# Kernel optimization log

Hardware: AMD Instinct MI355X
Metric: run time of the kernel (lower is better)

Reference implementation:

```python
import jax, jax.numpy as jnp
import numpy as np
from jax import lax

NUM_HEADS = 8


def setup_inputs() -> dict:
    key = jax.random.key(0)
    ks = jax.random.split(key, 6)
    B, L, Hd = 4, 4096, 512
    S = 45  # factor * ceil(ln(L)) = 5 * 9
    x = jax.random.normal(ks[0], (B, L, Hd), dtype=jnp.float32)
    scale = 1.0 / np.sqrt(Hd)
    Wq = jax.random.normal(ks[1], (Hd, Hd), dtype=jnp.float32) * scale
    Wk = jax.random.normal(ks[2], (Hd, Hd), dtype=jnp.float32) * scale
    Wv = jax.random.normal(ks[3], (Hd, Hd), dtype=jnp.float32) * scale
    Wo = jax.random.normal(ks[4], (Hd, Hd), dtype=jnp.float32) * scale
    index_sample = jax.random.randint(ks[5], (L, S), 0, L, dtype=jnp.int32)
    return {"x": x, "Wq": Wq, "Wk": Wk, "Wv": Wv, "Wo": Wo,
            "index_sample": index_sample}


def reference(x, Wq, Wk, Wv, Wo, index_sample):
    B, L, Hd = x.shape
    H = NUM_HEADS
    D = Hd // H
    S = index_sample.shape[1]
    u = S  # n_top active queries = factor*ceil(ln(L))

    def split_heads(t):  # [B,L,Hd] -> [B,H,L,D]
        return t.reshape(B, L, H, D).transpose(0, 2, 1, 3)

    q = split_heads(x @ Wq)
    k = split_heads(x @ Wk)
    v = split_heads(x @ Wv)

    scale = 1.0 / jnp.sqrt(jnp.asarray(D, dtype=x.dtype))

    # sampled key gather: [B,H,L,S,D]
    K_samp = k[:, :, index_sample, :]
    # sampled scores per query: [B,H,L,S]
    QK_samp = jnp.einsum('bhld,bhlsd->bhls', q, K_samp)
    # sparsity measurement: max - mean over sampled keys
    M = QK_samp.max(axis=-1) - QK_samp.mean(axis=-1)  # [B,H,L]
    _, top_idx = lax.top_k(M, u)                      # [B,H,u]

    # full attention only for active queries
    Qr = jnp.take_along_axis(q, top_idx[..., None], axis=2)   # [B,H,u,D]
    scores = jnp.einsum('bhud,bhld->bhul', Qr, k) * scale     # [B,H,u,L]
    attn = jax.nn.softmax(scores, axis=-1)
    ctx_sel = jnp.einsum('bhul,bhld->bhud', attn, v)          # [B,H,u,D]

    # inactive queries get mean(V); scatter active results in
    context = jnp.broadcast_to(v.mean(axis=2, keepdims=True), (B, H, L, D))
    b_idx = jnp.arange(B)[:, None, None]
    h_idx = jnp.arange(H)[None, :, None]
    context = context.at[b_idx, h_idx, top_idx].set(ctx_sel)

    out = context.transpose(0, 2, 1, 3).reshape(B, L, Hd) @ Wo
    return out
```

## Files before the change

### kernel.cpp

```cpp
#include <hip/hip_runtime.h>
#include <cmath>

#define SS 45
#define FSPLIT 16

typedef __attribute__((ext_vector_type(8))) _Float16 half8;
typedef __attribute__((ext_vector_type(4))) float float4v;
typedef __attribute__((ext_vector_type(8))) unsigned short ushort8v;

__device__ inline unsigned short f16b(float f) {
    union { _Float16 h; unsigned short u; } c;
    c.h = (_Float16)f;
    return c.u;
}
__device__ inline float f16back(unsigned short u) {
    union { _Float16 h; unsigned short u; } c;
    c.u = u;
    return (float)c.h;
}

__device__ __forceinline__ void async16(const void* g, void* l) {
    __builtin_amdgcn_global_load_lds(
        (const __attribute__((address_space(1))) void*)g,
        (__attribute__((address_space(3))) void*)l, 16, 0, 0);
}

template <int CTRL>
__device__ __forceinline__ float dppadd(float v) {
    int x = __builtin_amdgcn_mov_dpp(__float_as_int(v), CTRL, 0xF, 0xF, true);
    return v + __int_as_float(x);
}
template <int CTRL>
__device__ __forceinline__ float dppmax(float v) {
    int x = __builtin_amdgcn_mov_dpp(__float_as_int(v), CTRL, 0xF, 0xF, true);
    return fmaxf(v, __int_as_float(x));
}

__device__ __forceinline__ unsigned int fmono(float f) {
    unsigned int u = __float_as_uint(f);
    return (u & 0x80000000u) ? ~u : (u | 0x80000000u);
}

__global__ __launch_bounds__(256) void convW_kernel(
    const float* __restrict__ Wq, const float* __restrict__ Wk, const float* __restrict__ Wv,
    unsigned short* __restrict__ WTh, unsigned short* __restrict__ WTl,
    float* __restrict__ vmp)
{
    int bid = blockIdx.x;
    if (bid < 768) {
        int zy = bid >> 8;
        int bxy = bid & 255;
        const float* W = (zy == 0) ? Wq : (zy == 1) ? Wk : Wv;
        unsigned short* th = WTh + (size_t)zy * 262144;
        unsigned short* tl = WTl + (size_t)zy * 262144;
        __shared__ float t[32][33];
        int bx = bxy & 15, by = bxy >> 4;
        int tx = threadIdx.x & 31, ty = threadIdx.x >> 5;
        for (int i = ty; i < 32; i += 8) t[i][tx] = W[(size_t)(by * 32 + i) * 512 + bx * 32 + tx];
        __syncthreads();
        for (int i = ty; i < 32; i += 8) {
            float f = t[tx][i];
            unsigned short h = f16b(f);
            unsigned short lo = f16b(f - f16back(h));
            th[(size_t)(bx * 32 + i) * 512 + by * 32 + tx] = h;
            tl[(size_t)(bx * 32 + i) * 512 + by * 32 + tx] = lo;
        }
    } else {
        for (int i = threadIdx.x; i < 2048; i += 256) vmp[i] = 0.f;
    }
}

__global__ __launch_bounds__(512, 2) void qkv8_kernel(
    const float* __restrict__ X,
    const unsigned short* __restrict__ WTh, const unsigned short* __restrict__ WTl,
    float* __restrict__ Q, float* __restrict__ K, float* __restrict__ V,
    float* __restrict__ vmp)
{
    __shared__ unsigned short lds[73728];

    int wave = threadIdx.x >> 6;
    int lane = threadIdx.x & 63;
    int m0blk = blockIdx.x * 256;
    int n0blk = blockIdx.y * 128;
    int fr = lane & 15;
    int C = lane >> 4;
    int srow = lane >> 2;
    int sslot = lane & 3;
    int mrb = (wave >> 1) * 64;
    int nrb = (wave & 1) * 64;

    const unsigned short* gbB[5];
    gbB[0] = WTh;
    gbB[1] = WTl;
    gbB[2] = WTh + 262144;
    gbB[3] = WTl + 262144;
    gbB[4] = WTh + 524288;

    int rloc0 = wave * 32 + srow;
    int rloc1 = wave * 32 + 16 + srow;
    int Cp0 = sslot ^ ((rloc0 >> 1) & 3);
    int Cp1 = sslot ^ ((rloc1 >> 1) & 3);
    const float* xr0 = X + (size_t)(m0blk + rloc0) * 512 + Cp0 * 8;
    const float* xr1 = X + (size_t)(m0blk + rloc1) * 512 + Cp1 * 8;

    float4v accq[4][4], acck[4][4], accv[4][4];
    #pragma unroll
    for (int i = 0; i < 4; i++)
        #pragma unroll
        for (int j = 0; j < 4; j++) {
            accq[i][j] = (float4v){0.f, 0.f, 0.f, 0.f};
            acck[i][j] = (float4v){0.f, 0.f, 0.f, 0.f};
            accv[i][j] = (float4v){0.f, 0.f, 0.f, 0.f};
        }

    auto stageB = [&](int buf, int k0) {
        int rloc = wave * 16 + srow;
        int Cp = sslot ^ ((rloc >> 1) & 3);
        #pragma unroll
        for (int t = 0; t < 5; t++) {
            const unsigned short* g = gbB[t] + (size_t)(n0blk + rloc) * 512 + k0 + Cp * 8;
            async16(g, lds + buf * 36864 + 16384 + t * 4096 + wave * 512);
        }
    };

    float4 xv[2][2];
    auto loadX = [&](int k0) {
        xv[0][0] = *(const float4*)(xr0 + k0);
        xv[0][1] = *(const float4*)(xr0 + k0 + 4);
        xv[1][0] = *(const float4*)(xr1 + k0);
        xv[1][1] = *(const float4*)(xr1 + k0 + 4);
    };
    auto writeA = [&](int buf) {
        #pragma unroll
        for (int inst = 0; inst < 2; inst++) {
            const float* f = (const float*)&xv[inst][0];
            ushort8v hv, lv;
            #pragma unroll
            for (int e = 0; e < 8; e++) {
                unsigned short h = f16b(f[e]);
                hv[e] = h;
                lv[e] = f16b(f[e] - f16back(h));
            }
            unsigned short* dsth = lds + buf * 36864 + (wave * 32 + inst * 16) * 32 + lane * 8;
            *(ushort8v*)dsth = hv;
            *(ushort8v*)(dsth + 8192) = lv;
        }
    };

    loadX(0);
    stageB(0, 0);
    writeA(0);
    asm volatile("s_waitcnt vmcnt(0)" ::: "memory");
    asm volatile("s_waitcnt lgkmcnt(0)" ::: "memory");
    __builtin_amdgcn_s_barrier();

    for (int kk = 0; kk < 16; kk++) {
        const unsigned short* Lb = lds + (kk & 1) * 36864;
        int nbuf = (kk + 1) & 1;
        int nk0 = (kk + 1) * 32;

        if (kk < 15) {
            loadX(nk0);
            stageB(nbuf, nk0);
        }

        half8 A_h[4], A_l[4];
        #pragma unroll
        for (int i = 0; i < 4; i++) {
            int R = mrb + i * 16 + fr;
            int sl = C ^ ((R >> 1) & 3);
            A_h[i] = *(const half8*)(Lb + R * 32 + sl * 8);
            A_l[i] = *(const half8*)(Lb + 8192 + R * 32 + sl * 8);
        }
        #pragma unroll
        for (int j = 0; j < 4; j++) {
            int R = nrb + j * 16 + fr;
            int sl = C ^ ((R >> 1) & 3);
            int off = R * 32 + sl * 8;
            half8 Bqh = *(const half8*)(Lb + 16384 + off);
            half8 Bql = *(const half8*)(Lb + 20480 + off);
            half8 Bkh = *(const half8*)(Lb + 24576 + off);
            half8 Bkl = *(const half8*)(Lb + 28672 + off);
            half8 Bvh = *(const half8*)(Lb + 32768 + off);
            #pragma unroll
            for (int i = 0; i < 4; i++) {
                accq[i][j] = __builtin_amdgcn_mfma_f32_16x16x32_f16(A_h[i], Bqh, accq[i][j], 0, 0, 0);
                accq[i][j] = __builtin_amdgcn_mfma_f32_16x16x32_f16(A_h[i], Bql, accq[i][j], 0, 0, 0);
                accq[i][j] = __builtin_amdgcn_mfma_f32_16x16x32_f16(A_l[i], Bqh, accq[i][j], 0, 0, 0);
                acck[i][j] = __builtin_amdgcn_mfma_f32_16x16x32_f16(A_h[i], Bkh, acck[i][j], 0, 0, 0);
                acck[i][j] = __builtin_amdgcn_mfma_f32_16x16x32_f16(A_h[i], Bkl, acck[i][j], 0, 0, 0);
                acck[i][j] = __builtin_amdgcn_mfma_f32_16x16x32_f16(A_l[i], Bkh, acck[i][j], 0, 0, 0);
                accv[i][j] = __builtin_amdgcn_mfma_f32_16x16x32_f16(A_h[i], Bvh, accv[i][j], 0, 0, 0);
            }
        }

        if (kk < 15) {
            writeA(nbuf);
            asm volatile("s_waitcnt vmcnt(0)" ::: "memory");
            asm volatile("s_waitcnt lgkmcnt(0)" ::: "memory");
            __builtin_amdgcn_s_barrier();
        }
    }

    int hh = n0blk + nrb;
    int hd = hh >> 6;
    int bb0 = (m0blk + mrb) >> 12;
    {
        float cs[4];
        #pragma unroll
        for (int j = 0; j < 4; j++) {
            float s = 0.f;
            #pragma unroll
            for (int i = 0; i < 4; i++)
                #pragma unroll
                for (int r = 0; r < 4; r++) s += accv[i][j][r];
            s += __shfl_xor(s, 16, 64);
            s += __shfl_xor(s, 32, 64);
            cs[j] = s;
        }
        if (C == 0) {
            #pragma unroll
            for (int j = 0; j < 4; j++)
                atomicAdd(vmp + ((size_t)(bb0 * 8 + hd) * 64) + j * 16 + fr, cs[j]);
        }
    }

    int rbase = C * 4;
    int m0 = m0blk + mrb;
    #pragma unroll
    for (int i = 0; i < 4; i++)
        #pragma unroll
        for (int r = 0; r < 4; r++) {
            int rg = m0 + i * 16 + rbase + r;
            int bb = rg >> 12, l = rg & 4095;
            size_t rowoff = ((size_t)(bb * 8 + hd) * 4096 + l) * 64;
            #pragma unroll
            for (int j = 0; j < 4; j++) Q[rowoff + j * 16 + fr] = accq[i][j][r];
            #pragma unroll
            for (int j = 0; j < 4; j++) K[rowoff + j * 16 + fr] = acck[i][j][r];
            #pragma unroll
            for (int j = 0; j < 4; j++) V[rowoff + j * 16 + fr] = accv[i][j][r];
        }
}

__global__ __launch_bounds__(256) void m_kernel(
    const float* __restrict__ Q, const float* __restrict__ K,
    const int* __restrict__ idx, float* __restrict__ M)
{
    int inst = blockIdx.x * 4 + (threadIdx.x >> 6);
    int lane = threadIdx.x & 63;
    int g = lane >> 3;
    int t = lane & 7;
    int bh = inst >> 12;
    int l = inst & 4095;
    float4 qa = *(const float4*)(Q + (size_t)inst * 64 + t * 4);
    float4 qb = *(const float4*)(Q + (size_t)inst * 64 + 32 + t * 4);
    const float* kb = K + (size_t)bh * 4096 * 64;
    const int* irow = idx + (size_t)l * SS;
    int jv[6];
    #pragma unroll
    for (int it = 0; it < 6; it++) {
        int s = it * 8 + g;
        jv[it] = irow[(it == 5 && g >= 5) ? 0 : s];
    }
    float4 kva[6], kvb[6];
    #pragma unroll
    for (int it = 0; it < 6; it++) {
        kva[it] = *(const float4*)(kb + (size_t)jv[it] * 64 + t * 4);
        kvb[it] = *(const float4*)(kb + (size_t)jv[it] * 64 + 32 + t * 4);
    }
    float maxv = -1e30f, sum = 0.f, p0 = 0.f;
    #pragma unroll
    for (int it = 0; it < 6; it++) {
        float p = qa.x * kva[it].x;
        p = fmaf(qa.y, kva[it].y, p);
        p = fmaf(qa.z, kva[it].z, p);
        p = fmaf(qa.w, kva[it].w, p);
        p = fmaf(qb.x, kvb[it].x, p);
        p = fmaf(qb.y, kvb[it].y, p);
        p = fmaf(qb.z, kvb[it].z, p);
        p = fmaf(qb.w, kvb[it].w, p);
        p = dppadd<0xB1>(p);
        p = dppadd<0x4E>(p);
        p = dppadd<0x141>(p);
        if (it == 0) p0 = p;
        maxv = fmaxf(maxv, p);
        sum += p;
    }
    maxv = dppmax<0x128>(maxv);
    maxv = fmaxf(maxv, __shfl_xor(maxv, 16, 64));
    maxv = fmaxf(maxv, __shfl_xor(maxv, 32, 64));
    sum = dppadd<0x128>(sum);
    sum += __shfl_xor(sum, 16, 64);
    sum += __shfl_xor(sum, 32, 64);
    float p0b = __shfl(p0, 0, 64);
    if (lane == 0) M[inst] = maxv - (sum - 3.f * p0b) * (1.f / 45.f);
}

__global__ __launch_bounds__(256) void topk_local_kernel(
    const float* __restrict__ M, unsigned long long* __restrict__ cand)
{
    int chunk = blockIdx.x;
    int bh = chunk >> 3, c = chunk & 7;
    __shared__ unsigned long long keys[512];
    int tid = threadIdx.x;
    for (int i = tid; i < 512; i += 256) {
        int l = c * 512 + i;
        unsigned int u = fmono(M[(size_t)bh * 4096 + l]);
        keys[i] = ((unsigned long long)u << 32) | (unsigned int)(4095 - l);
    }
    __syncthreads();
    for (int k = 2; k <= 512; k <<= 1)
        for (int j = k >> 1; j > 0; j >>= 1) {
            for (int i0 = tid; i0 < 512; i0 += 256) {
                int ixj = i0 ^ j;
                if (ixj > i0) {
                    unsigned long long a = keys[i0], b = keys[ixj];
                    bool asc = (i0 & k) != 0;
                    if (asc ? (a > b) : (a < b)) { keys[i0] = b; keys[ixj] = a; }
                }
            }
            __syncthreads();
        }
    if (tid < SS) cand[(size_t)chunk * SS + tid] = keys[tid];
}

__global__ __launch_bounds__(256) void topk_merge_base_kernel(
    const unsigned long long* __restrict__ cand, int* __restrict__ tidx,
    const float* __restrict__ vmp, const float* __restrict__ Wo,
    float* __restrict__ vmean, float* __restrict__ base)
{
    int bid = blockIdx.x;
    int tid = threadIdx.x;
    if (bid < 32) {
        __shared__ unsigned long long keys[512];
        for (int i = tid; i < 512; i += 256) {
            unsigned long long v = 0ull;
            if (i < 8 * SS) {
                int cc = i / SS, r = i - cc * SS;
                v = cand[((size_t)bid * 8 + cc) * SS + r];
            }
            keys[i] = v;
        }
        __syncthreads();
        for (int k = 2; k <= 512; k <<= 1)
            for (int j = k >> 1; j > 0; j >>= 1) {
                for (int i0 = tid; i0 < 512; i0 += 256) {
                    int ixj = i0 ^ j;
                    if (ixj > i0) {
                        unsigned long long a = keys[i0], b = keys[ixj];
                        bool asc = (i0 & k) != 0;
                        if (asc ? (a > b) : (a < b)) { keys[i0] = b; keys[ixj] = a; }
                    }
                }
                __syncthreads();
            }
        if (tid < SS) tidx[bid * SS + tid] = 4095 - (int)(keys[tid] & 0xFFFFFFFFu);
    } else {
        int b = bid - 32;
        __shared__ float vmS[512];
        for (int i = tid; i < 512; i += 256) {
            float s = vmp[(size_t)b * 512 + i] * (1.f / 4096.f);
            vmS[i] = s;
            vmean[(size_t)b * 512 + i] = s;
        }
        __syncthreads();
        for (int jj = tid; jj < 512; jj += 256) {
            float s = 0.f;
            for (int i = 0; i < 512; i++) s += vmS[i] * Wo[(size_t)i * 512 + jj];
            base[(size_t)b * 512 + jj] = s;
        }
    }
}

__global__ __launch_bounds__(256) void attn_fill_kernel(
    const float* __restrict__ Q, const float* __restrict__ K, const float* __restrict__ V,
    const int* __restrict__ tidx,
    float* __restrict__ Opart, float* __restrict__ mpart, float* __restrict__ lpart,
    const float4* __restrict__ base4, float4* __restrict__ out4)
{
    int bid = blockIdx.x;
    if (bid >= 512) {
        int i = (bid - 512) * 256 + threadIdx.x;
        int b = i >> 19;
        int j4 = i & 127;
        out4[i] = base4[b * 128 + j4];
        return;
    }
    int split = bid & 15;
    int bh = bid >> 4;
    int L0 = split * (4096 / FSPLIT);

    __shared__ float Qs[48][68];
    __shared__ float Ks[64][68];
    __shared__ float Vs[64][68];
    __shared__ float Ps[48][68];
    __shared__ int tS[48];

    int tid = threadIdx.x;
    int lane = tid & 63, w = tid >> 6;
    if (tid < 48) tS[tid] = (tid < SS) ? tidx[bh * SS + tid] : 0;
    __syncthreads();
    for (int u = w; u < 48; u += 4)
        Qs[u][lane] = Q[((size_t)bh * 4096 + tS[u]) * 64 + lane];

    int ug = tid >> 4, lg = tid & 15;
    float mrun[4], lrun[4], O[4][4];
    #pragma unroll
    for (int i = 0; i < 4; i++) {
        mrun[i] = -1e30f; lrun[i] = 0.f;
        #pragma unroll
        for (int j = 0; j < 4; j++) O[i][j] = 0.f;
    }

    for (int tt = 0; tt < 4096 / FSPLIT / 64; tt++) {
        int lbase = L0 + tt * 64;
        if (tt > 0) __syncthreads();
        for (int r = w; r < 64; r += 4) {
            Ks[r][lane] = K[((size_t)bh * 4096 + lbase + r) * 64 + lane];
            Vs[r][lane] = V[((size_t)bh * 4096 + lbase + r) * 64 + lane];
        }
        __syncthreads();

        if (tid < 192) {
            float acc[4][4];
            #pragma unroll
            for (int i = 0; i < 4; i++)
                #pragma unroll
                for (int j = 0; j < 4; j++) acc[i][j] = 0.f;
            for (int d0 = 0; d0 < 64; d0 += 4) {
                float4 a[4], b[4];
                #pragma unroll
                for (int i = 0; i < 4; i++) a[i] = *(float4*)&Qs[ug * 4 + i][d0];
                #pragma unroll
                for (int j = 0; j < 4; j++) b[j] = *(float4*)&Ks[lg * 4 + j][d0];
                #pragma unroll
                for (int i = 0; i < 4; i++)
                    #pragma unroll
                    for (int j = 0; j < 4; j++)
                        acc[i][j] += a[i].x * b[j].x + a[i].y * b[j].y + a[i].z * b[j].z + a[i].w * b[j].w;
            }
            #pragma unroll
            for (int i = 0; i < 4; i++) {
                #pragma unroll
                for (int j = 0; j < 4; j++) acc[i][j] *= 0.125f;
                float tm = fmaxf(fmaxf(acc[i][0], acc[i][1]), fmaxf(acc[i][2], acc[i][3]));
                tm = fmaxf(tm, __shfl_xor(tm, 1, 64));
                tm = fmaxf(tm, __shfl_xor(tm, 2, 64));
                tm = fmaxf(tm, __shfl_xor(tm, 4, 64));
                tm = fmaxf(tm, __shfl_xor(tm, 8, 64));
                float nm = fmaxf(mrun[i], tm);
                float corr = __expf(mrun[i] - nm);
                float rs = 0.f;
                #pragma unroll
                for (int j = 0; j < 4; j++) {
                    float p = __expf(acc[i][j] - nm);
                    Ps[ug * 4 + i][lg * 4 + j] = p;
                    rs += p;
                }
                rs += __shfl_xor(rs, 1, 64);
                rs += __shfl_xor(rs, 2, 64);
                rs += __shfl_xor(rs, 4, 64);
                rs += __shfl_xor(rs, 8, 64);
                lrun[i] = lrun[i] * corr + rs;
                mrun[i] = nm;
                #pragma unroll
                for (int j = 0; j < 4; j++) O[i][j] *= corr;
            }
        }
        __syncthreads();

        if (tid < 192) {
            for (int l0 = 0; l0 < 64; l0 += 4) {
                float4 vr[4];
                #pragma unroll
                for (int r = 0; r < 4; r++) vr[r] = *(float4*)&Vs[l0 + r][lg * 4];
                #pragma unroll
                for (int i = 0; i < 4; i++) {
                    float4 pv = *(float4*)&Ps[ug * 4 + i][l0];
                    #pragma unroll
                    for (int j = 0; j < 4; j++) {
                        float vj0 = (&vr[0].x)[j], vj1 = (&vr[1].x)[j];
                        float vj2 = (&vr[2].x)[j], vj3 = (&vr[3].x)[j];
                        O[i][j] = fmaf(pv.x, vj0, fmaf(pv.y, vj1, fmaf(pv.z, vj2, fmaf(pv.w, vj3, O[i][j]))));
                    }
                }
            }
        }
    }

    if (tid < 192) {
        #pragma unroll
        for (int i = 0; i < 4; i++) {
            int u = ug * 4 + i;
            if (u < SS) {
                size_t pbase = ((size_t)(bh * FSPLIT + split) * SS + u);
                if (lg == 0) { mpart[pbase] = mrun[i]; lpart[pbase] = lrun[i]; }
                #pragma unroll
                for (int j = 0; j < 4; j++)
                    Opart[pbase * 64 + lg * 4 + j] = O[i][j];
            }
        }
    }
}

__global__ __launch_bounds__(256) void combine_kernel(
    const float* __restrict__ Opart, const float* __restrict__ mpart, const float* __restrict__ lpart,
    const float* __restrict__ vmean, const float* __restrict__ Wo,
    const int* __restrict__ tidx, float* __restrict__ out)
{
    int rr = blockIdx.x;
    int bh = rr / SS, u = rr % SS;
    int h = bh & 7, b = bh >> 3;
    __shared__ float dS[64];
    int tid = threadIdx.x;
    if (tid < 64) {
        float m = -1e30f;
        #pragma unroll
        for (int s = 0; s < FSPLIT; s++)
            m = fmaxf(m, mpart[(size_t)(bh * FSPLIT + s) * SS + u]);
        float den = 0.f, num = 0.f;
        #pragma unroll
        for (int s = 0; s < FSPLIT; s++) {
            size_t pbase = (size_t)(bh * FSPLIT + s) * SS + u;
            float wgt = __expf(mpart[pbase] - m);
            den += wgt * lpart[pbase];
            num += wgt * Opart[pbase * 64 + tid];
        }
        dS[tid] = num / den - vmean[(size_t)bh * 64 + tid];
    }
    __syncthreads();
    int l = tidx[rr];
    float* orow = out + ((size_t)b * 4096 + l) * 512;
    for (int j = tid; j < 512; j += 256) {
        float s = 0.f;
        #pragma unroll
        for (int dd = 0; dd < 64; dd++) s += dS[dd] * Wo[(size_t)(h * 64 + dd) * 512 + j];
        atomicAdd(orow + j, s);
    }
}

extern "C" void kernel_launch(void* const* d_in, const int* in_sizes, int n_in,
                              void* d_out, int out_size, void* d_ws, size_t ws_size,
                              hipStream_t stream)
{
    const float* x  = (const float*)d_in[0];
    const float* Wq = (const float*)d_in[1];
    const float* Wk = (const float*)d_in[2];
    const float* Wv = (const float*)d_in[3];
    const float* Wo = (const float*)d_in[4];
    const int*  idx = (const int*)d_in[5];
    float* out = (float*)d_out;

    float* W = (float*)d_ws;
    float* Q = W;
    float* K = W + 8388608;
    float* V = W + 16777216;
    unsigned short* WTh = (unsigned short*)(W + 33554432);
    unsigned short* WTl = (unsigned short*)(W + 33947648);
    float* vmp = W + 34340864;

    float* Mv    = W + 25165824;
    float* Opart = W + 25296896;
    float* mpart = W + 26771456;
    float* lpart = W + 26794496;
    float* vmean = W + 33439744;
    float* base  = W + 33441792;
    int*   tidx  = (int*)(W + 33443840);
    unsigned long long* cand = (unsigned long long*)(W + 33445280);

    convW_kernel<<<769, 256, 0, stream>>>(Wq, Wk, Wv, WTh, WTl, vmp);
    qkv8_kernel<<<dim3(64, 4), 512, 0, stream>>>(x, WTh, WTl, Q, K, V, vmp);
    m_kernel<<<32768, 256, 0, stream>>>(Q, K, idx, Mv);
    topk_local_kernel<<<256, 256, 0, stream>>>(Mv, cand);
    topk_merge_base_kernel<<<36, 256, 0, stream>>>(cand, tidx, vmp, Wo, vmean, base);
    attn_fill_kernel<<<512 + 8192, 256, 0, stream>>>(Q, K, V, tidx, Opart, mpart, lpart,
                                                     (const float4*)base, (float4*)out);
    combine_kernel<<<1440, 256, 0, stream>>>(Opart, mpart, lpart, vmean, Wo, tidx, out);
}
```

Baseline: 399.7 us.

## Load X directly into MFMA registers and shrink QKV GEMM tile to 128 rows

Result: slower. 510.5 us (+27.7%).

```diff
diff --git a/kernel.cpp b/kernel.cpp
--- a/kernel.cpp
+++ b/kernel.cpp
@@ -70,17 +70,17 @@
     }
 }
 
-__global__ __launch_bounds__(512, 2) void qkv8_kernel(
+__global__ __launch_bounds__(256, 2) void qkv9_kernel(
     const float* __restrict__ X,
     const unsigned short* __restrict__ WTh, const unsigned short* __restrict__ WTl,
     float* __restrict__ Q, float* __restrict__ K, float* __restrict__ V,
     float* __restrict__ vmp)
 {
-    __shared__ unsigned short lds[73728];
+    __shared__ unsigned short lds[40960];
 
     int wave = threadIdx.x >> 6;
     int lane = threadIdx.x & 63;
-    int m0blk = blockIdx.x * 256;
+    int m0blk = blockIdx.x * 128;
     int n0blk = blockIdx.y * 128;
     int fr = lane & 15;
     int C = lane >> 4;
@@ -96,12 +96,10 @@
     gbB[3] = WTl + 262144;
     gbB[4] = WTh + 524288;
 
-    int rloc0 = wave * 32 + srow;
-    int rloc1 = wave * 32 + 16 + srow;
-    int Cp0 = sslot ^ ((rloc0 >> 1) & 3);
-    int Cp1 = sslot ^ ((rloc1 >> 1) & 3);
-    const float* xr0 = X + (size_t)(m0blk + rloc0) * 512 + Cp0 * 8;
-    const float* xr1 = X + (size_t)(m0blk + rloc1) * 512 + Cp1 * 8;
+    const float* xr0 = X + (size_t)(m0blk + mrb +  0 + fr) * 512 + C * 8;
+    const float* xr1 = X + (size_t)(m0blk + mrb + 16 + fr) * 512 + C * 8;
+    const float* xr2 = X + (size_t)(m0blk + mrb + 32 + fr) * 512 + C * 8;
+    const float* xr3 = X + (size_t)(m0blk + mrb + 48 + fr) * 512 + C * 8;
 
     float4v accq[4][4], acck[4][4], accv[4][4];
     #pragma unroll
@@ -114,89 +112,76 @@
         }
 
     auto stageB = [&](int buf, int k0) {
-        int rloc = wave * 16 + srow;
-        int Cp = sslot ^ ((rloc >> 1) & 3);
-        #pragma unroll
-        for (int t = 0; t < 5; t++) {
-            const unsigned short* g = gbB[t] + (size_t)(n0blk + rloc) * 512 + k0 + Cp * 8;
-            async16(g, lds + buf * 36864 + 16384 + t * 4096 + wave * 512);
-        }
+        #pragma unroll
+        for (int t = 0; t < 5; t++)
+            #pragma unroll
+            for (int inst = 0; inst < 2; inst++) {
+                int rloc = inst * 64 + wave * 16 + srow;
+                int Cp = sslot ^ ((rloc >> 1) & 3);
+                const unsigned short* g = gbB[t] + (size_t)(n0blk + rloc) * 512 + k0 + Cp * 8;
+                async16(g, lds + buf * 20480 + t * 4096 + (inst * 64 + wave * 16) * 32);
+            }
     };
 
-    float4 xv[2][2];
+    float4 xraw[4][2];
     auto loadX = [&](int k0) {
-        xv[0][0] = *(const float4*)(xr0 + k0);
-        xv[0][1] = *(const float4*)(xr0 + k0 + 4);
-        xv[1][0] = *(const float4*)(xr1 + k0);
-        xv[1][1] = *(const float4*)(xr1 + k0 + 4);
+        xraw[0][0] = *(const float4*)(xr0 + k0); xraw[0][1] = *(const float4*)(xr0 + k0 + 4);
+        xraw[1][0] = *(const float4*)(xr1 + k0); xraw[1][1] = *(const float4*)(xr1 + k0 + 4);
+        xraw[2][0] = *(const float4*)(xr2 + k0); xraw[2][1] = *(const float4*)(xr2 + k0 + 4);
+        xraw[3][0] = *(const float4*)(xr3 + k0); xraw[3][1] = *(const float4*)(xr3 + k0 + 4);
     };
-    auto writeA = [&](int buf) {
-        #pragma unroll
-        for (int inst = 0; inst < 2; inst++) {
-            const float* f = (const float*)&xv[inst][0];
-            ushort8v hv, lv;
+
+    stageB(0, 0);
+    loadX(0);
+    asm volatile("s_waitcnt vmcnt(8)" ::: "memory");
+    __builtin_amdgcn_s_barrier();
+
+    for (int kk = 0; kk < 16; kk++) {
+        const unsigned short* Lb = lds + (kk & 1) * 20480;
+        int nbuf = (kk + 1) & 1;
+        int nk0 = (kk + 1) * 32;
+
+        union { ushort8v u; half8 h; } Ah[4], Al[4];
+        #pragma unroll
+        for (int i = 0; i < 4; i++) {
+            const float* f = (const float*)&xraw[i][0];
             #pragma unroll
             for (int e = 0; e < 8; e++) {
                 unsigned short h = f16b(f[e]);
-                hv[e] = h;
-                lv[e] = f16b(f[e] - f16back(h));
-            }
-            unsigned short* dsth = lds + buf * 36864 + (wave * 32 + inst * 16) * 32 + lane * 8;
-            *(ushort8v*)dsth = hv;
-            *(ushort8v*)(dsth + 8192) = lv;
-        }
-    };
-
-    loadX(0);
-    stageB(0, 0);
-    writeA(0);
-    asm volatile("s_waitcnt vmcnt(0)" ::: "memory");
-    asm volatile("s_waitcnt lgkmcnt(0)" ::: "memory");
-    __builtin_amdgcn_s_barrier();
-
-    for (int kk = 0; kk < 16; kk++) {
-        const unsigned short* Lb = lds + (kk & 1) * 36864;
-        int nbuf = (kk + 1) & 1;
-        int nk0 = (kk + 1) * 32;
+                Ah[i].u[e] = h;
+                Al[i].u[e] = f16b(f[e] - f16back(h));
+            }
+        }
 
         if (kk < 15) {
+            stageB(nbuf, nk0);
             loadX(nk0);
-            stageB(nbuf, nk0);
-        }
-
-        half8 A_h[4], A_l[4];
-        #pragma unroll
-        for (int i = 0; i < 4; i++) {
-            int R = mrb + i * 16 + fr;
-            int sl = C ^ ((R >> 1) & 3);
-            A_h[i] = *(const half8*)(Lb + R * 32 + sl * 8);
-            A_l[i] = *(const half8*)(Lb + 8192 + R * 32 + sl * 8);
-        }
+        }
+
         #pragma unroll
         for (int j = 0; j < 4; j++) {
             int R = nrb + j * 16 + fr;
             int sl = C ^ ((R >> 1) & 3);
             int off = R * 32 + sl * 8;
-            half8 Bqh = *(const half8*)(Lb + 16384 + off);
-            half8 Bql = *(const half8*)(Lb + 20480 + off);
-            half8 Bkh = *(const half8*)(Lb + 24576 + off);
-            half8 Bkl = *(const half8*)(Lb + 28672 + off);
-            half8 Bvh = *(const half8*)(Lb + 32768 + off);
+            half8 Bqh = *(const half8*)(Lb + off);
+            half8 Bql = *(const half8*)(Lb + 4096 + off);
+            half8 Bkh = *(const half8*)(Lb + 8192 + off);
+            half8 Bkl = *(const half8*)(Lb + 12288 + off);
+            half8 Bvh = *(const half8*)(Lb + 16384 + off);
             #pragma unroll
             for (int i = 0; i < 4; i++) {
-                accq[i][j] = __builtin_amdgcn_mfma_f32_16x16x32_f16(A_h[i], Bqh, accq[i][j], 0, 0, 0);
-                accq[i][j] = __builtin_amdgcn_mfma_f32_16x16x32_f16(A_h[i], Bql, accq[i][j], 0, 0, 0);
-                accq[i][j] = __builtin_amdgcn_mfma_f32_16x16x32_f16(A_l[i], Bqh, accq[i][j], 0, 0, 0);
-                acck[i][j] = __builtin_amdgcn_mfma_f32_16x16x32_f16(A_h[i], Bkh, acck[i][j], 0, 0, 0);
-                acck[i][j] = __builtin_amdgcn_mfma_f32_16x16x32_f16(A_h[i], Bkl, acck[i][j], 0, 0, 0);
-                acck[i][j] = __builtin_amdgcn_mfma_f32_16x16x32_f16(A_l[i], Bkh, acck[i][j], 0, 0, 0);
-                accv[i][j] = __builtin_amdgcn_mfma_f32_16x16x32_f16(A_h[i], Bvh, accv[i][j], 0, 0, 0);
+                accq[i][j] = __builtin_amdgcn_mfma_f32_16x16x32_f16(Ah[i].h, Bqh, accq[i][j], 0, 0, 0);
+                accq[i][j] = __builtin_amdgcn_mfma_f32_16x16x32_f16(Ah[i].h, Bql, accq[i][j], 0, 0, 0);
+                accq[i][j] = __builtin_amdgcn_mfma_f32_16x16x32_f16(Al[i].h, Bqh, accq[i][j], 0, 0, 0);
+                acck[i][j] = __builtin_amdgcn_mfma_f32_16x16x32_f16(Ah[i].h, Bkh, acck[i][j], 0, 0, 0);
+                acck[i][j] = __builtin_amdgcn_mfma_f32_16x16x32_f16(Ah[i].h, Bkl, acck[i][j], 0, 0, 0);
+                acck[i][j] = __builtin_amdgcn_mfma_f32_16x16x32_f16(Al[i].h, Bkh, acck[i][j], 0, 0, 0);
+                accv[i][j] = __builtin_amdgcn_mfma_f32_16x16x32_f16(Ah[i].h, Bvh, accv[i][j], 0, 0, 0);
             }
         }
 
         if (kk < 15) {
-            writeA(nbuf);
-            asm volatile("s_waitcnt vmcnt(0)" ::: "memory");
+            asm volatile("s_waitcnt vmcnt(8)" ::: "memory");
             asm volatile("s_waitcnt lgkmcnt(0)" ::: "memory");
             __builtin_amdgcn_s_barrier();
         }
@@ -570,7 +555,7 @@
     unsigned long long* cand = (unsigned long long*)(W + 33445280);
 
     convW_kernel<<<769, 256, 0, stream>>>(Wq, Wk, Wv, WTh, WTl, vmp);
-    qkv8_kernel<<<dim3(64, 4), 512, 0, stream>>>(x, WTh, WTl, Q, K, V, vmp);
+    qkv9_kernel<<<dim3(128, 4), 256, 0, stream>>>(x, WTh, WTl, Q, K, V, vmp);
     m_kernel<<<32768, 256, 0, stream>>>(Q, K, idx, Mv);
     topk_local_kernel<<<256, 256, 0, stream>>>(Mv, cand);
     topk_merge_base_kernel<<<36, 256, 0, stream>>>(cand, tidx, vmp, Wo, vmean, base);
```
